# Performance work log

Hardware: AMD Instinct MI355X
Metric: run time of the kernel (lower is better)

Reference implementation:

```python
import jax, jax.numpy as jnp
import numpy as np

B = 16384      # batch
FEAT = 4096    # features
D = 64         # nearest_root_factors(4096) -> (64, 64)
BN_EPS = 1e-3


def setup_inputs() -> dict:
    key = jax.random.key(0)
    ks = jax.random.split(key, 9)
    stdv1 = 1.0 / np.sqrt(D)   # layer1: zero_initialization=False path
    stdv2 = 0.001              # layer2: zero_initialization=True path

    def u(k, shape, s):
        return jax.random.uniform(k, shape, minval=-s, maxval=s, dtype=jnp.float32)

    return {
        "inputs": jax.random.normal(ks[0], (B, FEAT), dtype=jnp.float32),
        "bn0_gamma": jnp.ones((FEAT,), jnp.float32),
        "bn0_beta": jnp.zeros((FEAT,), jnp.float32),
        "bn1_gamma": jnp.ones((FEAT,), jnp.float32),
        "bn1_beta": jnp.zeros((FEAT,), jnp.float32),
        # Kronecker layer 1 (left: weights (o2=input_dim1, o1=out_dim1); right: (d,d))
        "k1_lw": u(ks[1], (D, D), stdv1),
        "k1_lb": u(ks[2], (D, D), stdv1),
        "k1_rw": u(ks[3], (D, D), stdv1),
        "k1_rb": u(ks[4], (D, D), stdv1),
        # Kronecker layer 2 (zero-initialized)
        "k2_lw": u(ks[5], (D, D), stdv2),
        "k2_lb": u(ks[6], (D, D), stdv2),
        "k2_rw": u(ks[7], (D, D), stdv2),
        "k2_rb": u(ks[8], (D, D), stdv2),
    }


def _batch_norm(x, gamma, beta):
    # training-mode BN: biased batch statistics over the batch dim, eps=1e-3
    m = jnp.mean(x, axis=0)
    v = jnp.var(x, axis=0)
    return (x - m) * jax.lax.rsqrt(v + BN_EPS) * gamma + beta


def _kron_block(t, lw, lb, rw, rb):
    # KDLeftLayer: permute(matmul(permute(x,[0,2,1]), W),[0,2,1]) + b
    #   out[b,o,j] = sum_k x[b,k,j] * W[k,o]
    t = jnp.einsum("bkj,ko->boj", t, lw) + lb
    # KDRightLayer: x @ W + b
    t = jnp.matmul(t, rw) + rb
    return t


def reference(inputs, bn0_gamma, bn0_beta, bn1_gamma, bn1_beta,
              k1_lw, k1_lb, k1_rw, k1_rb, k2_lw, k2_lb, k2_rw, k2_rb):
    t = jax.nn.relu(_batch_norm(inputs, bn0_gamma, bn0_beta))
    t = t.reshape(-1, D, D)
    t = _kron_block(t, k1_lw, k1_lb, k1_rw, k1_rb).reshape(-1, FEAT)
    t = jax.nn.relu(_batch_norm(t, bn1_gamma, bn1_beta))
    # dropout p=0.0 -> identity
    t = t.reshape(-1, D, D)
    t = _kron_block(t, k2_lw, k2_lb, k2_rw, k2_rb).reshape(-1, FEAT)
    return inputs + t
```

## Files before the change

kernel.cpp:

```cpp
#include <hip/hip_runtime.h>

#define NROWS 16384
#define NFEAT 4096

typedef __attribute__((ext_vector_type(8))) short          bfrag8;
typedef __attribute__((ext_vector_type(4))) float          fvec4;
typedef __attribute__((ext_vector_type(4))) unsigned short usvec4;
typedef __attribute__((ext_vector_type(8))) unsigned short usvec8;

#define WS_P0   ((size_t)0)
#define WS_P1   ((size_t)16 << 20)
#define WS_SC0  ((size_t)48 << 20)
#define WS_SH0  (WS_SC0 + 16384)
#define WS_SC1  (WS_SC0 + 32768)
#define WS_SH1  (WS_SC0 + 49152)
#define WS_C1   (WS_SC0 + 65536)
#define WS_C2   (WS_SC0 + 81920)
#define WS_T1   ((size_t)64 << 20)

__device__ __forceinline__ unsigned short f2bf_bits(float f) {
  unsigned u = __builtin_bit_cast(unsigned, f);
  u += 0x7FFFu + ((u >> 16) & 1u);
  return (unsigned short)(u >> 16);
}
__device__ __forceinline__ float bf2f(unsigned short b) {
  return __builtin_bit_cast(float, ((unsigned)b) << 16);
}
__device__ __forceinline__ usvec4 pack4(fvec4 a) {
  usvec4 p;
#pragma unroll
  for (int e = 0; e < 4; ++e) p[e] = f2bf_bits(a[e]);
  return p;
}
__device__ __forceinline__ fvec4 unpack4(usvec4 p) {
  return fvec4{bf2f(p[0]), bf2f(p[1]), bf2f(p[2]), bf2f(p[3])};
}

__global__ __launch_bounds__(256) void k_bn0part(const float* __restrict__ x,
                                                 unsigned short* __restrict__ p0) {
  const int t = threadIdx.x, p = blockIdx.x;
  fvec4 s[4], sq[4];
#pragma unroll
  for (int q = 0; q < 4; ++q) { s[q] = fvec4{0.f,0.f,0.f,0.f}; sq[q] = s[q]; }
  for (int r = p * 16; r < p * 16 + 16; ++r) {
    const fvec4* row = (const fvec4*)(x + (size_t)r * NFEAT);
#pragma unroll
    for (int q = 0; q < 4; ++q) {
      fvec4 v = row[t + 256 * q];
      s[q] += v; sq[q] += v * v;
    }
  }
#pragma unroll
  for (int q = 0; q < 4; ++q) {
    int f0 = (t + 256 * q) * 4;
    *(usvec4*)(p0 + (size_t)p * 8192 + f0)        = pack4(s[q]);
    *(usvec4*)(p0 + (size_t)p * 8192 + 4096 + f0) = pack4(sq[q]);
  }
}

__device__ __forceinline__ void red_body(fvec4 (*red)[16][2],
                                         const unsigned short* __restrict__ parts,
                                         int nsets,
                                         const float* __restrict__ g,
                                         const float* __restrict__ bta,
                                         float* __restrict__ sc_out,
                                         float* __restrict__ sh_out, int j) {
  const int t = threadIdx.x;
  const int fc = t & 15, c = t >> 4;
  const int v = j * 64 + fc * 4;
  fvec4 s = fvec4{0.f,0.f,0.f,0.f}, q = s;
  for (int i = c; i < nsets; i += 16) {
    s += unpack4(*(const usvec4*)(parts + (size_t)i * 8192 + v));
    q += unpack4(*(const usvec4*)(parts + (size_t)i * 8192 + 4096 + v));
  }
  red[c][fc][0] = s; red[c][fc][1] = q;
  __syncthreads();
  if (c == 0) {
    fvec4 S = red[0][fc][0], Q = red[0][fc][1];
#pragma unroll
    for (int k = 1; k < 16; ++k) { S += red[k][fc][0]; Q += red[k][fc][1]; }
    fvec4 SC, SH;
    const float inv = 1.0f / NROWS;
#pragma unroll
    for (int e = 0; e < 4; ++e) {
      float mean = S[e] * inv;
      float var  = Q[e] * inv - mean * mean;
      float scv  = g[v + e] * rsqrtf(var + 1e-3f);
      SC[e] = scv; SH[e] = bta[v + e] - mean * scv;
    }
    *(fvec4*)(sc_out + v) = SC;
    *(fvec4*)(sh_out + v) = SH;
  }
}

__global__ __launch_bounds__(256) void k_prep0(const unsigned short* __restrict__ p0,
                                               const float* __restrict__ g0,
                                               const float* __restrict__ b0,
                                               float* __restrict__ sc0,
                                               float* __restrict__ sh0,
                                               const float* __restrict__ lb1,
                                               const float* __restrict__ rw1,
                                               const float* __restrict__ rb1,
                                               const float* __restrict__ lb2,
                                               const float* __restrict__ rw2,
                                               const float* __restrict__ rb2,
                                               float* __restrict__ c1,
                                               float* __restrict__ c2) {
  __shared__ fvec4 red[16][16][2];
  if (blockIdx.x < 64) {
    red_body(red, p0, 1024, g0, b0, sc0, sh0, blockIdx.x);
  } else {
    const int bb   = blockIdx.x - 64;
    const int idx  = (bb & 15) * 256 + threadIdx.x;
    const int part = bb >> 4;
    const float* lb = part ? lb2 : lb1;
    const float* rw = part ? rw2 : rw1;
    const float* rb = part ? rb2 : rb1;
    int r = idx >> 6, o = idx & 63;
    float acc = rb[o * 64 + r];
    for (int j = 0; j < 64; ++j) acc += lb[o * 64 + j] * rw[j * 64 + r];
    (part ? c2 : c1)[o * 64 + r] = acc;
  }
}

__global__ __launch_bounds__(256) void k_red1(const unsigned short* __restrict__ p1,
                                              const float* __restrict__ g1,
                                              const float* __restrict__ b1,
                                              float* __restrict__ sc1,
                                              float* __restrict__ sh1) {
  __shared__ fvec4 red[16][16][2];
  red_body(red, p1, 2048, g1, b1, sc1, sh1, blockIdx.x);
}

template <int LAYER, int RPBN>
__global__ __launch_bounds__(256) void k_kron(const float* __restrict__ x,
                                              const float* __restrict__ lw,
                                              const float* __restrict__ rw,
                                              const float* __restrict__ scv,
                                              const float* __restrict__ shv,
                                              const float* __restrict__ cn,
                                              unsigned short* __restrict__ t1,
                                              float* __restrict__ outf,
                                              unsigned short* __restrict__ p1) {
  __shared__ unsigned short vt[2][64 * 64];
  const int tid = threadIdx.x, bid = blockIdx.x;
  const int w = tid >> 6, l = tid & 63, m = l & 15, g = l >> 4;
  const int r0 = bid * RPBN;

  bfrag8 frw[4][2];
#pragma unroll
  for (int rt = 0; rt < 4; ++rt)
#pragma unroll
    for (int ks = 0; ks < 2; ++ks)
#pragma unroll
      for (int i = 0; i < 8; ++i)
        frw[rt][ks][i] = (short)f2bf_bits(rw[(ks * 32 + g * 8 + i) * 64 + rt * 16 + m]);

  bfrag8 flw[2];
#pragma unroll
  for (int ks = 0; ks < 2; ++ks)
#pragma unroll
    for (int i = 0; i < 8; ++i)
      flw[ks][i] = (short)f2bf_bits(lw[(ks * 32 + g * 8 + i) * 64 + w * 16 + m]);

  fvec4 cb[4];
#pragma unroll
  for (int rt = 0; rt < 4; ++rt)
    cb[rt] = *(const fvec4*)(cn + (w * 16 + m) * 64 + rt * 16 + g * 4);

  float sc[2][8], sh[2][8];
#pragma unroll
  for (int ks = 0; ks < 2; ++ks) {
    int f = (w * 16 + m) * 64 + ks * 32 + g * 8;
    fvec4 a0 = *(const fvec4*)(scv + f), a1 = *(const fvec4*)(scv + f + 4);
    fvec4 h0 = *(const fvec4*)(shv + f), h1 = *(const fvec4*)(shv + f + 4);
#pragma unroll
    for (int e = 0; e < 4; ++e) {
      sc[ks][e] = a0[e]; sc[ks][4 + e] = a1[e];
      sh[ks][e] = h0[e]; sh[ks][4 + e] = h1[e];
    }
  }

  fvec4 s1[4], q1[4];
#pragma unroll
  for (int rt = 0; rt < 4; ++rt) { s1[rt] = fvec4{0.f,0.f,0.f,0.f}; q1[rt] = s1[rt]; }

  fvec4  pfx[2][4];
  usvec8 pft[2][2];
  fvec4  pfr[2][4];

  if constexpr (LAYER == 1) {
    const fvec4* px = (const fvec4*)(x + (size_t)r0 * NFEAT + (w * 16 + m) * 64);
    pfx[0][0] = px[g * 2];     pfx[0][1] = px[g * 2 + 1];
    pfx[0][2] = px[8 + g * 2]; pfx[0][3] = px[8 + g * 2 + 1];
  } else {
    const usvec8* pt = (const usvec8*)(t1 + (size_t)r0 * NFEAT);
    pft[0][0] = pt[(w * 16 + m) * 8 + g];
    pft[0][1] = pt[(w * 16 + m) * 8 + 4 + g];
    const fvec4* pin = (const fvec4*)(x + (size_t)r0 * NFEAT);
#pragma unroll
    for (int rt = 0; rt < 4; ++rt)
      pfr[0][rt] = pin[((w * 16 + m) * 64 + rt * 16 + g * 4) >> 2];
  }

#pragma unroll
  for (int rr = 0; rr < RPBN; ++rr) {
    const int b = r0 + rr;
    const int cur = rr & 1, nxt = cur ^ 1;

    if (rr + 1 < RPBN) {
      if constexpr (LAYER == 1) {
        const fvec4* px = (const fvec4*)(x + (size_t)(b + 1) * NFEAT + (w * 16 + m) * 64);
        pfx[nxt][0] = px[g * 2];     pfx[nxt][1] = px[g * 2 + 1];
        pfx[nxt][2] = px[8 + g * 2]; pfx[nxt][3] = px[8 + g * 2 + 1];
      } else {
        const usvec8* pt = (const usvec8*)(t1 + (size_t)(b + 1) * NFEAT);
        pft[nxt][0] = pt[(w * 16 + m) * 8 + g];
        pft[nxt][1] = pt[(w * 16 + m) * 8 + 4 + g];
        const fvec4* pin = (const fvec4*)(x + (size_t)(b + 1) * NFEAT);
#pragma unroll
        for (int rt = 0; rt < 4; ++rt)
          pfr[nxt][rt] = pin[((w * 16 + m) * 64 + rt * 16 + g * 4) >> 2];
      }
    }

    bfrag8 fa[2];
    if constexpr (LAYER == 1) {
#pragma unroll
      for (int ks = 0; ks < 2; ++ks) {
        fvec4 v0 = pfx[cur][ks * 2], v1 = pfx[cur][ks * 2 + 1];
        float yv[8] = {v0[0], v0[1], v0[2], v0[3], v1[0], v1[1], v1[2], v1[3]};
#pragma unroll
        for (int i = 0; i < 8; ++i) {
          float y = fmaxf(yv[i] * sc[ks][i] + sh[ks][i], 0.f);
          fa[ks][i] = (short)f2bf_bits(y);
        }
      }
    } else {
#pragma unroll
      for (int ks = 0; ks < 2; ++ks) {
        usvec8 tv = pft[cur][ks];
#pragma unroll
        for (int i = 0; i < 8; ++i) {
          float y = fmaxf(bf2f(tv[i]) * sc[ks][i] + sh[ks][i], 0.f);
          fa[ks][i] = (short)f2bf_bits(y);
        }
      }
    }

#pragma unroll
    for (int rt = 0; rt < 4; ++rt) {
      fvec4 va = fvec4{0.f,0.f,0.f,0.f};
      va = __builtin_amdgcn_mfma_f32_16x16x32_bf16(fa[0], frw[rt][0], va, 0, 0, 0);
      va = __builtin_amdgcn_mfma_f32_16x16x32_bf16(fa[1], frw[rt][1], va, 0, 0, 0);
      int ridx = rt * 16 + m;
      int chunk = 2 * w + (g >> 1);
      int byte = ridx * 128 + ((chunk ^ (ridx & 7)) << 4) + ((g & 1) * 8);
      *(usvec4*)((char*)(&vt[cur][0]) + byte) = pack4(va);
    }

    asm volatile("s_waitcnt lgkmcnt(0)\n\ts_barrier" ::: "memory");

    fvec4 za[4];
#pragma unroll
    for (int rt = 0; rt < 4; ++rt) za[rt] = fvec4{0.f,0.f,0.f,0.f};
#pragma unroll
    for (int ks = 0; ks < 2; ++ks) {
#pragma unroll
      for (int rt = 0; rt < 4; ++rt) {
        int ridx = rt * 16 + m;
        int byte = ridx * 128 + (((ks * 4 + g) ^ (ridx & 7)) << 4);
        bfrag8 av = *(const bfrag8*)((const char*)(&vt[cur][0]) + byte);
        za[rt] = __builtin_amdgcn_mfma_f32_16x16x32_bf16(av, flw[ks], za[rt], 0, 0, 0);
      }
    }

    if constexpr (LAYER == 1) {
#pragma unroll
      for (int rt = 0; rt < 4; ++rt) {
        fvec4 z = za[rt] + cb[rt];
        s1[rt] += z; q1[rt] += z * z;
        *(usvec4*)(t1 + (size_t)b * NFEAT +
                   (w * 16 + m) * 64 + rt * 16 + g * 4) = pack4(z);
      }
    } else {
      fvec4* pout = (fvec4*)(outf + (size_t)b * NFEAT);
#pragma unroll
      for (int rt = 0; rt < 4; ++rt) {
        int fi = ((w * 16 + m) * 64 + rt * 16 + g * 4) >> 2;
        pout[fi] = pfr[cur][rt] + za[rt] + cb[rt];
      }
    }
  }

  if constexpr (LAYER == 1) {
#pragma unroll
    for (int rt = 0; rt < 4; ++rt) {
      int vf = (w * 16 + m) * 64 + rt * 16 + g * 4;
      *(usvec4*)(p1 + (size_t)bid * 8192 + vf)        = pack4(s1[rt]);
      *(usvec4*)(p1 + (size_t)bid * 8192 + 4096 + vf) = pack4(q1[rt]);
    }
  }
}

extern "C" void kernel_launch(void* const* d_in, const int* in_sizes, int n_in,
                              void* d_out, int out_size, void* d_ws, size_t ws_size,
                              hipStream_t stream) {
  (void)in_sizes; (void)n_in; (void)out_size; (void)ws_size;
  const float* x    = (const float*)d_in[0];
  const float* g0   = (const float*)d_in[1];
  const float* b0   = (const float*)d_in[2];
  const float* g1   = (const float*)d_in[3];
  const float* b1   = (const float*)d_in[4];
  const float* k1lw = (const float*)d_in[5];
  const float* k1lb = (const float*)d_in[6];
  const float* k1rw = (const float*)d_in[7];
  const float* k1rb = (const float*)d_in[8];
  const float* k2lw = (const float*)d_in[9];
  const float* k2lb = (const float*)d_in[10];
  const float* k2rw = (const float*)d_in[11];
  const float* k2rb = (const float*)d_in[12];
  char* ws = (char*)d_ws;

  unsigned short* p0  = (unsigned short*)(ws + WS_P0);
  unsigned short* p1  = (unsigned short*)(ws + WS_P1);
  unsigned short* t1  = (unsigned short*)(ws + WS_T1);
  float* sc0 = (float*)(ws + WS_SC0);
  float* sh0 = (float*)(ws + WS_SH0);
  float* sc1 = (float*)(ws + WS_SC1);
  float* sh1 = (float*)(ws + WS_SH1);
  float* c1  = (float*)(ws + WS_C1);
  float* c2  = (float*)(ws + WS_C2);

  k_bn0part<<<1024, 256, 0, stream>>>(x, p0);
  k_prep0<<<96, 256, 0, stream>>>(p0, g0, b0, sc0, sh0,
                                  k1lb, k1rw, k1rb, k2lb, k2rw, k2rb, c1, c2);
  k_kron<1, 8><<<NROWS / 8, 256, 0, stream>>>(x, k1lw, k1rw, sc0, sh0, c1,
                                              t1, nullptr, p1);
  k_red1<<<64, 256, 0, stream>>>(p1, g1, b1, sc1, sh1);
  k_kron<2, 8><<<NROWS / 8, 256, 0, stream>>>(x, k2lw, k2rw, sc1, sh1, c2,
                                              t1, (float*)d_out, nullptr);
}
```

Measured before the change: 388.9 us.

## Stage a bf16 copy of inputs during BN0 stats and read it in both Kronecker passes

The BN0 statistics kernel now also writes a bf16 copy of the input matrix into workspace. Both Kronecker kernels read that half-width copy instead of the fp32 input, for the layer-1 activations and for the layer-2 residual. The prefetch is also reworked to keep two rows in flight. This cuts total HBM traffic, since the fp32 input is read once instead of three times, at the cost of an extra bf16 write. The risk is that the final residual `inputs + t` now uses bf16-rounded inputs, which lowers output precision and could exceed the accuracy tolerance.

```diff
diff --git a/kernel.cpp b/kernel.cpp
--- a/kernel.cpp
+++ b/kernel.cpp
@@ -17,6 +17,7 @@
 #define WS_C1   (WS_SC0 + 65536)
 #define WS_C2   (WS_SC0 + 81920)
 #define WS_T1   ((size_t)64 << 20)
+#define WS_XB   ((size_t)192 << 20)
 
 __device__ __forceinline__ unsigned short f2bf_bits(float f) {
   unsigned u = __builtin_bit_cast(unsigned, f);
@@ -37,17 +38,20 @@
 }
 
 __global__ __launch_bounds__(256) void k_bn0part(const float* __restrict__ x,
-                                                 unsigned short* __restrict__ p0) {
+                                                 unsigned short* __restrict__ p0,
+                                                 unsigned short* __restrict__ xb) {
   const int t = threadIdx.x, p = blockIdx.x;
   fvec4 s[4], sq[4];
 #pragma unroll
   for (int q = 0; q < 4; ++q) { s[q] = fvec4{0.f,0.f,0.f,0.f}; sq[q] = s[q]; }
   for (int r = p * 16; r < p * 16 + 16; ++r) {
     const fvec4* row = (const fvec4*)(x + (size_t)r * NFEAT);
+    usvec4* xrow = (usvec4*)(xb + (size_t)r * NFEAT);
 #pragma unroll
     for (int q = 0; q < 4; ++q) {
       fvec4 v = row[t + 256 * q];
       s[q] += v; sq[q] += v * v;
+      xrow[t + 256 * q] = pack4(v);
     }
   }
 #pragma unroll
@@ -133,7 +137,7 @@
 }
 
 template <int LAYER, int RPBN>
-__global__ __launch_bounds__(256) void k_kron(const float* __restrict__ x,
+__global__ __launch_bounds__(256) void k_kron(const unsigned short* __restrict__ xb,
                                               const float* __restrict__ lw,
                                               const float* __restrict__ rw,
                                               const float* __restrict__ scv,
@@ -146,6 +150,7 @@
   const int tid = threadIdx.x, bid = blockIdx.x;
   const int w = tid >> 6, l = tid & 63, m = l & 15, g = l >> 4;
   const int r0 = bid * RPBN;
+  const unsigned short* asrc = (LAYER == 1) ? xb : t1;
 
   bfrag8 frw[4][2];
 #pragma unroll
@@ -185,67 +190,46 @@
 #pragma unroll
   for (int rt = 0; rt < 4; ++rt) { s1[rt] = fvec4{0.f,0.f,0.f,0.f}; q1[rt] = s1[rt]; }
 
-  fvec4  pfx[2][4];
-  usvec8 pft[2][2];
-  fvec4  pfr[2][4];
-
-  if constexpr (LAYER == 1) {
-    const fvec4* px = (const fvec4*)(x + (size_t)r0 * NFEAT + (w * 16 + m) * 64);
-    pfx[0][0] = px[g * 2];     pfx[0][1] = px[g * 2 + 1];
-    pfx[0][2] = px[8 + g * 2]; pfx[0][3] = px[8 + g * 2 + 1];
-  } else {
-    const usvec8* pt = (const usvec8*)(t1 + (size_t)r0 * NFEAT);
-    pft[0][0] = pt[(w * 16 + m) * 8 + g];
-    pft[0][1] = pt[(w * 16 + m) * 8 + 4 + g];
-    const fvec4* pin = (const fvec4*)(x + (size_t)r0 * NFEAT);
-#pragma unroll
-    for (int rt = 0; rt < 4; ++rt)
-      pfr[0][rt] = pin[((w * 16 + m) * 64 + rt * 16 + g * 4) >> 2];
+  usvec8 pfa[2][2];
+  usvec4 pfr[2][4];
+
+  {
+    const usvec8* pt0 = (const usvec8*)(asrc + (size_t)r0 * NFEAT);
+    const usvec8* pt1 = (const usvec8*)(asrc + (size_t)(r0 + 1) * NFEAT);
+    pfa[0][0] = pt0[(w * 16 + m) * 8 + g];
+    pfa[0][1] = pt0[(w * 16 + m) * 8 + 4 + g];
+    pfa[1][0] = pt1[(w * 16 + m) * 8 + g];
+    pfa[1][1] = pt1[(w * 16 + m) * 8 + 4 + g];
+    if constexpr (LAYER == 2) {
+#pragma unroll
+      for (int rt = 0; rt < 4; ++rt) {
+        int off = (w * 16 + m) * 64 + rt * 16 + g * 4;
+        pfr[0][rt] = *(const usvec4*)(xb + (size_t)r0 * NFEAT + off);
+        pfr[1][rt] = *(const usvec4*)(xb + (size_t)(r0 + 1) * NFEAT + off);
+      }
+    }
   }
 
 #pragma unroll
   for (int rr = 0; rr < RPBN; ++rr) {
     const int b = r0 + rr;
-    const int cur = rr & 1, nxt = cur ^ 1;
-
-    if (rr + 1 < RPBN) {
-      if constexpr (LAYER == 1) {
-        const fvec4* px = (const fvec4*)(x + (size_t)(b + 1) * NFEAT + (w * 16 + m) * 64);
-        pfx[nxt][0] = px[g * 2];     pfx[nxt][1] = px[g * 2 + 1];
-        pfx[nxt][2] = px[8 + g * 2]; pfx[nxt][3] = px[8 + g * 2 + 1];
-      } else {
-        const usvec8* pt = (const usvec8*)(t1 + (size_t)(b + 1) * NFEAT);
-        pft[nxt][0] = pt[(w * 16 + m) * 8 + g];
-        pft[nxt][1] = pt[(w * 16 + m) * 8 + 4 + g];
-        const fvec4* pin = (const fvec4*)(x + (size_t)(b + 1) * NFEAT);
-#pragma unroll
-        for (int rt = 0; rt < 4; ++rt)
-          pfr[nxt][rt] = pin[((w * 16 + m) * 64 + rt * 16 + g * 4) >> 2];
-      }
-    }
+    const int cur = rr & 1;
 
     bfrag8 fa[2];
-    if constexpr (LAYER == 1) {
-#pragma unroll
-      for (int ks = 0; ks < 2; ++ks) {
-        fvec4 v0 = pfx[cur][ks * 2], v1 = pfx[cur][ks * 2 + 1];
-        float yv[8] = {v0[0], v0[1], v0[2], v0[3], v1[0], v1[1], v1[2], v1[3]};
-#pragma unroll
-        for (int i = 0; i < 8; ++i) {
-          float y = fmaxf(yv[i] * sc[ks][i] + sh[ks][i], 0.f);
-          fa[ks][i] = (short)f2bf_bits(y);
-        }
-      }
-    } else {
-#pragma unroll
-      for (int ks = 0; ks < 2; ++ks) {
-        usvec8 tv = pft[cur][ks];
-#pragma unroll
-        for (int i = 0; i < 8; ++i) {
-          float y = fmaxf(bf2f(tv[i]) * sc[ks][i] + sh[ks][i], 0.f);
-          fa[ks][i] = (short)f2bf_bits(y);
-        }
-      }
+#pragma unroll
+    for (int ks = 0; ks < 2; ++ks) {
+      usvec8 tv = pfa[cur][ks];
+#pragma unroll
+      for (int i = 0; i < 8; ++i) {
+        float y = fmaxf(bf2f(tv[i]) * sc[ks][i] + sh[ks][i], 0.f);
+        fa[ks][i] = (short)f2bf_bits(y);
+      }
+    }
+
+    if (rr + 2 < RPBN) {
+      const usvec8* pt = (const usvec8*)(asrc + (size_t)(b + 2) * NFEAT);
+      pfa[cur][0] = pt[(w * 16 + m) * 8 + g];
+      pfa[cur][1] = pt[(w * 16 + m) * 8 + 4 + g];
     }
 
 #pragma unroll
@@ -288,7 +272,14 @@
 #pragma unroll
       for (int rt = 0; rt < 4; ++rt) {
         int fi = ((w * 16 + m) * 64 + rt * 16 + g * 4) >> 2;
-        pout[fi] = pfr[cur][rt] + za[rt] + cb[rt];
+        pout[fi] = unpack4(pfr[cur][rt]) + za[rt] + cb[rt];
+      }
+      if (rr + 2 < RPBN) {
+#pragma unroll
+        for (int rt = 0; rt < 4; ++rt) {
+          int off = (w * 16 + m) * 64 + rt * 16 + g * 4;
+          pfr[cur][rt] = *(const usvec4*)(xb + (size_t)(b + 2) * NFEAT + off);
+        }
       }
     }
   }
@@ -325,6 +316,7 @@
   unsigned short* p0  = (unsigned short*)(ws + WS_P0);
   unsigned short* p1  = (unsigned short*)(ws + WS_P1);
   unsigned short* t1  = (unsigned short*)(ws + WS_T1);
+  unsigned short* xb  = (unsigned short*)(ws + WS_XB);
   float* sc0 = (float*)(ws + WS_SC0);
   float* sh0 = (float*)(ws + WS_SH0);
   float* sc1 = (float*)(ws + WS_SC1);
@@ -332,12 +324,12 @@
   float* c1  = (float*)(ws + WS_C1);
   float* c2  = (float*)(ws + WS_C2);
 
-  k_bn0part<<<1024, 256, 0, stream>>>(x, p0);
+  k_bn0part<<<1024, 256, 0, stream>>>(x, p0, xb);
   k_prep0<<<96, 256, 0, stream>>>(p0, g0, b0, sc0, sh0,
                                   k1lb, k1rw, k1rb, k2lb, k2rw, k2rb, c1, c2);
-  k_kron<1, 8><<<NROWS / 8, 256, 0, stream>>>(x, k1lw, k1rw, sc0, sh0, c1,
+  k_kron<1, 8><<<NROWS / 8, 256, 0, stream>>>(xb, k1lw, k1rw, sc0, sh0, c1,
                                               t1, nullptr, p1);
   k_red1<<<64, 256, 0, stream>>>(p1, g1, b1, sc1, sh1);
-  k_kron<2, 8><<<NROWS / 8, 256, 0, stream>>>(x, k2lw, k2rw, sc1, sh1, c2,
+  k_kron<2, 8><<<NROWS / 8, 256, 0, stream>>>(xb, k2lw, k2rw, sc1, sh1, c2,
                                               t1, (float*)d_out, nullptr);
 }
```

Measured after the change: 383.2 us. No clear change (-1.5%).
